# Kernel optimization log

Hardware: AMD Instinct MI355X
Metric: run time of the kernel (lower is better)

## Reference

```python
import jax, jax.numpy as jnp
import numpy as np

E = 2  # expand_ratio


def _linear_scan(u, a):
    """h_t = a_t * h_{t-1} + u_t along axis 0, h_{-1}=0. Parallel associative scan."""
    def comb(x, y):
        a1, b1 = x
        a2, b2 = y
        return a2 * a1, a2 * b1 + b2
    _, h = jax.lax.associative_scan(comb, (a, u), axis=0)
    return h


def setup_inputs() -> dict:
    key = jax.random.key(0)
    ks = jax.random.split(key, 8)
    n, b, d = 2048, 4, 1024
    s = 1.0 / np.sqrt(d)
    return {
        "x": jax.random.normal(ks[0], (n, b, d), jnp.float32),
        "lower_bound": jax.random.uniform(ks[1], (d,), jnp.float32),
        "W_in": jax.random.normal(ks[2], (d, 3 * d), jnp.float32) * s,
        "b_in": jnp.zeros((3 * d,), jnp.float32),
        "W_out": jax.random.normal(ks[3], (d, d), jnp.float32) * s,
        "b_out": jnp.zeros((d,), jnp.float32),
        "gamma": jnp.ones((d,), jnp.float32),
        "beta": jnp.zeros((d,), jnp.float32),
    }


def reference(x, lower_bound, W_in, b_in, W_out, b_out, gamma, beta):
    n, b, d = x.shape
    h = d // E
    feat = x @ W_in + b_in                      # (n,b,3d)
    inp, og, fg = jnp.split(feat, 3, axis=-1)
    inp = jax.nn.silu(inp)
    og = jax.nn.sigmoid(og)
    fg = jax.nn.sigmoid(fg)
    # reshape (h d) -> h, d=E
    inp = inp.reshape(n, b, h, E)
    og = og.reshape(n, b, h, E)
    fg = fg.reshape(n, b, h, E)
    lb = lower_bound.reshape(h, E)
    lam = lb + (1.0 - lb) * fg                  # (n,b,h,E)
    # outer-product input: (1-lam) outer inp over the E dims -> (n,b,h,E,E)
    u = jnp.einsum('nbhd,nbhe->nbhde', 1.0 - lam, inp)
    a = jnp.broadcast_to(lam[..., None], u.shape)
    u = u.reshape(n, b, h * E * E)
    a = a.reshape(n, b, h * E * E)
    state_fwd = _linear_scan(u, a)
    state_rev = jnp.flip(_linear_scan(jnp.flip(u, 0), jnp.flip(a, 0)), 0)
    state = (state_fwd + state_rev).reshape(n, b, h, E, E)
    out = jnp.einsum('nbhde,nbhd->nbhe', state, og).reshape(n, b, d)
    # layernorm over last dim
    mu = jnp.mean(out, axis=-1, keepdims=True)
    var = jnp.var(out, axis=-1, keepdims=True)
    out = (out - mu) * jax.lax.rsqrt(var + 1e-5) * gamma + beta
    return out @ W_out + b_out
```

## Files before the change

kernel.cpp:

```cpp
#include <hip/hip_runtime.h>

typedef __bf16 bf16x8 __attribute__((ext_vector_type(8)));
typedef float floatx4 __attribute__((ext_vector_type(4)));

#define NCH 128
#define CLEN 16

__device__ __forceinline__ unsigned short f2bf(float f) {
  unsigned int u = __builtin_bit_cast(unsigned int, f);
  u += 0x7fff + ((u >> 16) & 1);
  return (unsigned short)(u >> 16);
}
__device__ __forceinline__ float bf2f(unsigned short u) {
  unsigned int v = (unsigned int)u << 16;
  return __builtin_bit_cast(float, v);
}
__device__ __forceinline__ float bf2f_lo(unsigned int u) {
  return __builtin_bit_cast(float, u << 16);
}
__device__ __forceinline__ float bf2f_hi(unsigned int u) {
  return __builtin_bit_cast(float, u & 0xffff0000u);
}

__device__ __forceinline__ void async_copy16(const void* g, void* l) {
  __builtin_amdgcn_global_load_lds(
      (const __attribute__((address_space(1))) unsigned int*)g,
      (__attribute__((address_space(3))) unsigned int*)l, 16, 0, 0);
}

__global__ void cast_x_kernel(const float* __restrict__ in, unsigned short* __restrict__ out) {
  int i = blockIdx.x * blockDim.x + threadIdx.x;
  float4 v = ((const float4*)in)[i];
  ushort4 o;
  o.x = f2bf(v.x); o.y = f2bf(v.y); o.z = f2bf(v.z); o.w = f2bf(v.w);
  ((ushort4*)out)[i] = o;
}

__global__ void tcast2_kernel(const float* __restrict__ Win, unsigned short* __restrict__ winT,
                              const float* __restrict__ Wout, unsigned short* __restrict__ woutT) {
  __shared__ float tile[32][33];
  int bx = blockIdx.x;
  const float* W;
  unsigned short* WT;
  int ncols, n0;
  if (bx < 96) { W = Win; WT = winT; ncols = 3072; n0 = bx * 32; }
  else { W = Wout; WT = woutT; ncols = 1024; n0 = (bx - 96) * 32; }
  int k0 = blockIdx.y * 32;
  int tx = threadIdx.x, ty = threadIdx.y;
  tile[ty][tx] = W[(size_t)(k0 + ty) * ncols + n0 + tx];
  __syncthreads();
  WT[(size_t)(n0 + ty) * 1024 + k0 + tx] = f2bf(tile[tx][ty]);
}

template <int EPI>
__global__ __launch_bounds__(256) void gemm_kernel(
    const unsigned short* __restrict__ A, const unsigned short* __restrict__ BT,
    const float* __restrict__ bias, const float* __restrict__ lb,
    float* __restrict__ outf,
    unsigned short* __restrict__ o_inp, unsigned short* __restrict__ o_og,
    unsigned short* __restrict__ o_om) {
  __shared__ alignas(16) char smem_raw[17408];
  unsigned short* As = (unsigned short*)smem_raw;
  unsigned short* Bs = As + 128 * 32;
  const int m0 = blockIdx.x * 128, n0 = blockIdx.y * 128;
  const int tid = threadIdx.x;
  const int lane = tid & 63, wave = tid >> 6;
  const int wm = (wave >> 1) * 64, wn = (wave & 1) * 64;
  const int mrow = lane & 15, q = lane >> 4;
  const int qsw = q ^ ((mrow >> 1) & 3);
  floatx4 acc[4][4] = {};
  const int r0 = wave * 32;
  const int srow = r0 + (lane >> 2);
  const int qs = (lane & 3) ^ ((srow >> 1) & 3);
  const unsigned short* gA0 = A + (size_t)(m0 + srow) * 1024 + qs * 8;
  const unsigned short* gA1 = gA0 + (size_t)16 * 1024;
  const unsigned short* gB0 = BT + (size_t)(n0 + srow) * 1024 + qs * 8;
  const unsigned short* gB1 = gB0 + (size_t)16 * 1024;
  unsigned short* lA0 = &As[r0 * 32];
  unsigned short* lA1 = &As[(r0 + 16) * 32];
  unsigned short* lB0 = &Bs[r0 * 32];
  unsigned short* lB1 = &Bs[(r0 + 16) * 32];
  for (int kt = 0; kt < 1024; kt += 32) {
    __syncthreads();
    async_copy16(gA0, lA0);
    async_copy16(gA1, lA1);
    async_copy16(gB0, lB0);
    async_copy16(gB1, lB1);
    gA0 += 32; gA1 += 32; gB0 += 32; gB1 += 32;
    __syncthreads();
    bf16x8 af[4], bf[4];
#pragma unroll
    for (int i = 0; i < 4; i++) af[i] = *(const bf16x8*)&As[(wm + i * 16 + mrow) * 32 + qsw * 8];
#pragma unroll
    for (int j = 0; j < 4; j++) bf[j] = *(const bf16x8*)&Bs[(wn + j * 16 + mrow) * 32 + qsw * 8];
#pragma unroll
    for (int i = 0; i < 4; i++)
#pragma unroll
      for (int j = 0; j < 4; j++)
        acc[i][j] = __builtin_amdgcn_mfma_f32_16x16x32_bf16(af[i], bf[j], acc[i][j], 0, 0, 0);
  }
  const int er = tid >> 3;
  const int ec = (tid & 7) * 16;
  const int rgbase = m0 + (er & 15) + (er >> 4) * 64;
  const int lr = (wm ? 16 : 0) + q * 4;
  float bi[4];
  int cidx[4];
#pragma unroll
  for (int j = 0; j < 4; j++) {
    cidx[j] = n0 + wn + j * 16 + mrow;
    bi[j] = bias[cidx[j]];
  }
  if (EPI == 1) {
    unsigned short* Cs = (unsigned short*)smem_raw;
    const int seg = n0 >> 10;
    unsigned short* dst = (seg == 0) ? o_inp : (seg == 1) ? o_og : o_om;
    float Lv[4];
    if (seg == 2) {
#pragma unroll
      for (int j = 0; j < 4; j++) Lv[j] = lb[cidx[j] & 1023];
    }
#pragma unroll
    for (int i = 0; i < 4; i++) {
      __syncthreads();
#pragma unroll
      for (int j = 0; j < 4; j++) {
        const int lc = wn + j * 16 + mrow;
#pragma unroll
        for (int g = 0; g < 4; g++) {
          float v = acc[i][j][g] + bi[j];
          unsigned short ob;
          if (seg == 0) { float s = 1.f / (1.f + __expf(-v)); ob = f2bf(v * s); }
          else if (seg == 1) { float s = 1.f / (1.f + __expf(-v)); ob = f2bf(s); }
          else { float sm = 1.f / (1.f + __expf(v)); ob = f2bf((1.f - Lv[j]) * sm); }
          Cs[(lr + g) * 136 + lc] = ob;
        }
      }
      __syncthreads();
      uint4 v0 = *(uint4*)&Cs[er * 136 + ec];
      uint4 v1 = *(uint4*)&Cs[er * 136 + ec + 8];
      size_t ro = (size_t)(rgbase + i * 16) * 1024 + (n0 & 1023) + ec;
      *(uint4*)&dst[ro] = v0;
      *(uint4*)&dst[ro + 8] = v1;
    }
  } else {
    float* Cf = (float*)smem_raw;
#pragma unroll
    for (int i = 0; i < 4; i++) {
      __syncthreads();
#pragma unroll
      for (int j = 0; j < 4; j++) {
        const int lc = wn + j * 16 + mrow;
#pragma unroll
        for (int g = 0; g < 4; g++) Cf[(lr + g) * 132 + lc] = acc[i][j][g] + bi[j];
      }
      __syncthreads();
      size_t ro = (size_t)(rgbase + i * 16) * 1024 + n0 + ec;
#pragma unroll
      for (int k = 0; k < 4; k++) {
        float4 v = *(float4*)&Cf[er * 132 + ec + k * 4];
        *(float4*)&outf[ro + k * 4] = v;
      }
    }
  }
}

__global__ __launch_bounds__(512, 2) void gemm1_kernel(
    const unsigned short* __restrict__ A, const unsigned short* __restrict__ BT,
    const float* __restrict__ bias, const float* __restrict__ lb,
    unsigned short* __restrict__ o_inp, unsigned short* __restrict__ o_og,
    unsigned short* __restrict__ o_om) {
  __shared__ alignas(16) char smem[131072];
  const int orig = blockIdx.x;
  const int wg = (orig & 7) * 48 + (orig >> 3);
  const int m0 = (wg & 31) << 8;
  const int n0 = (wg >> 5) << 8;
  const int tid = threadIdx.x;
  const int lane = tid & 63, wave = tid >> 6;
  const int wm = wave >> 2, wn = wave & 3;
  const int srow = tid >> 3;
  const int sq = (tid & 7) ^ (srow & 7);
  const unsigned short* gA = A + (size_t)(m0 + srow) * 1024 + sq * 8;
  const unsigned short* gB = BT + (size_t)(n0 + srow) * 1024 + sq * 8;
  char* lw = smem + wave * 1024;
  const int aro = (wm * 128 + (lane & 15)) * 128;
  const int bro = (wn * 64 + (lane & 15)) * 128;
  const int qs0 = ((lane >> 4) ^ (lane & 7)) * 16;
  const int qs1 = ((4 + (lane >> 4)) ^ (lane & 7)) * 16;

  floatx4 acc[8][4] = {};
  bf16x8 aF[4][2], bF[4][2];

#define STG(lofs, gh, kk)                                \
  do {                                                   \
    const unsigned short* _g = (gh) + (size_t)(kk) * 64; \
    async_copy16(_g, lw + (lofs));                       \
    async_copy16(_g + 65536, lw + (lofs) + 8192);        \
  } while (0)
#define RA(base, mh, i, s) \
  (*(const bf16x8*)(smem + (base) + aro + (mh) * 8192 + (i) * 2048 + ((s) ? qs1 : qs0)))
#define RB(base, j, s) \
  (*(const bf16x8*)(smem + (base) + bro + (j) * 2048 + ((s) ? qs1 : qs0)))
#define BAR __builtin_amdgcn_s_barrier()
#define LGKM0 asm volatile("s_waitcnt lgkmcnt(0)" ::: "memory")
#define VM4 asm volatile("s_waitcnt vmcnt(4)" ::: "memory")
#define MM(d, a, b) d = __builtin_amdgcn_mfma_f32_16x16x32_bf16(a, b, d, 0, 0, 0)

  STG(65536, gB, 0);
  STG(65536 + 16384, gB + 131072, 0);
  STG(0, gA, 0);
  STG(0 + 16384, gA + 131072, 0);
  STG(98304, gB, 1);
  STG(98304 + 16384, gB + 131072, 1);
  VM4;
  BAR;

#pragma unroll 1
  for (int it = 0; it < 8; ++it) {
    const int t0 = 2 * it;
    const int kA1 = t0 + 1;
    const int kN2 = (t0 + 2 > 15) ? 15 : t0 + 2;
    const int kN3 = (t0 + 3 > 15) ? 15 : t0 + 3;
#pragma unroll
    for (int i = 0; i < 4; i++) { aF[i][0] = RA(0, 0, i, 0); aF[i][1] = RA(0, 0, i, 1); }
#pragma unroll
    for (int j = 0; j < 2; j++) { bF[j][0] = RB(65536, j, 0); bF[j][1] = RB(65536, j, 1); }
    STG(32768, gA, kA1);
    BAR; LGKM0;
    __builtin_amdgcn_s_setprio(1);
#pragma unroll
    for (int i = 0; i < 4; i++)
#pragma unroll
      for (int j = 0; j < 2; j++) { MM(acc[i][j], aF[i][0], bF[j][0]); MM(acc[i][j], aF[i][1], bF[j][1]); }
    __builtin_amdgcn_s_setprio(0);
    BAR;
#pragma unroll
    for (int j = 2; j < 4; j++) { bF[j][0] = RB(65536, j, 0); bF[j][1] = RB(65536, j, 1); }
    STG(32768 + 16384, gA + 131072, kA1);
    BAR; LGKM0;
    __builtin_amdgcn_s_setprio(1);
#pragma unroll
    for (int i = 0; i < 4; i++)
#pragma unroll
      for (int j = 2; j < 4; j++) { MM(acc[i][j], aF[i][0], bF[j][0]); MM(acc[i][j], aF[i][1], bF[j][1]); }
    __builtin_amdgcn_s_setprio(0);
    BAR;
#pragma unroll
    for (int i = 0; i < 4; i++) { aF[i][0] = RA(0, 1, i, 0); aF[i][1] = RA(0, 1, i, 1); }
    STG(65536, gB, kN2);
    BAR; LGKM0;
    __builtin_amdgcn_s_setprio(1);
#pragma unroll
    for (int i = 0; i < 4; i++)
#pragma unroll
      for (int j = 0; j < 2; j++) { MM(acc[4 + i][j], aF[i][0], bF[j][0]); MM(acc[4 + i][j], aF[i][1], bF[j][1]); }
    __builtin_amdgcn_s_setprio(0);
    BAR;
    STG(65536 + 16384, gB + 131072, kN2);
    BAR;
    __builtin_amdgcn_s_setprio(1);
#pragma unroll
    for (int i = 0; i < 4; i++)
#pragma unroll
      for (int j = 2; j < 4; j++) { MM(acc[4 + i][j], aF[i][0], bF[j][0]); MM(acc[4 + i][j], aF[i][1], bF[j][1]); }
    __builtin_amdgcn_s_setprio(0);
    VM4;
    BAR;
#pragma unroll
    for (int i = 0; i < 4; i++) { aF[i][0] = RA(32768, 0, i, 0); aF[i][1] = RA(32768, 0, i, 1); }
#pragma unroll
    for (int j = 0; j < 2; j++) { bF[j][0] = RB(98304, j, 0); bF[j][1] = RB(98304, j, 1); }
    STG(0, gA, kN2);
    BAR; LGKM0;
    __builtin_amdgcn_s_setprio(1);
#pragma unroll
    for (int i = 0; i < 4; i++)
#pragma unroll
      for (int j = 0; j < 2; j++) { MM(acc[i][j], aF[i][0], bF[j][0]); MM(acc[i][j], aF[i][1], bF[j][1]); }
    __builtin_amdgcn_s_setprio(0);
    BAR;
#pragma unroll
    for (int j = 2; j < 4; j++) { bF[j][0] = RB(98304, j, 0); bF[j][1] = RB(98304, j, 1); }
    STG(16384, gA + 131072, kN2);
    BAR; LGKM0;
    __builtin_amdgcn_s_setprio(1);
#pragma unroll
    for (int i = 0; i < 4; i++)
#pragma unroll
      for (int j = 2; j < 4; j++) { MM(acc[i][j], aF[i][0], bF[j][0]); MM(acc[i][j], aF[i][1], bF[j][1]); }
    __builtin_amdgcn_s_setprio(0);
    BAR;
#pragma unroll
    for (int i = 0; i < 4; i++) { aF[i][0] = RA(32768, 1, i, 0); aF[i][1] = RA(32768, 1, i, 1); }
    STG(98304, gB, kN3);
    BAR; LGKM0;
    __builtin_amdgcn_s_setprio(1);
#pragma unroll
    for (int i = 0; i < 4; i++)
#pragma unroll
      for (int j = 0; j < 2; j++) { MM(acc[4 + i][j], aF[i][0], bF[j][0]); MM(acc[4 + i][j], aF[i][1], bF[j][1]); }
    __builtin_amdgcn_s_setprio(0);
    BAR;
    STG(98304 + 16384, gB + 131072, kN3);
    BAR;
    __builtin_amdgcn_s_setprio(1);
#pragma unroll
    for (int i = 0; i < 4; i++)
#pragma unroll
      for (int j = 2; j < 4; j++) { MM(acc[4 + i][j], aF[i][0], bF[j][0]); MM(acc[4 + i][j], aF[i][1], bF[j][1]); }
    __builtin_amdgcn_s_setprio(0);
    VM4;
    BAR;
  }
#undef STG
#undef RA
#undef RB
#undef BAR
#undef LGKM0
#undef VM4
#undef MM

  asm volatile("s_waitcnt vmcnt(0) lgkmcnt(0)" ::: "memory");
  const int seg = n0 >> 10;
  unsigned short* dst = (seg == 0) ? o_inp : (seg == 1) ? o_og : o_om;
  unsigned short* Cs = (unsigned short*)smem;
  float bi[4], Lv[4];
#pragma unroll
  for (int j = 0; j < 4; j++) {
    const int c = n0 + wn * 64 + j * 16 + (lane & 15);
    bi[j] = bias[c];
    Lv[j] = (seg == 2) ? lb[c & 1023] : 0.f;
  }
  const int lrw = wm * 16 + (lane >> 4) * 4;
  const int lcw = wn * 64 + (lane & 15);
  const int er = tid >> 4, ec = (tid & 15) * 16;
  const int growb = m0 + (er >> 4) * 128 + (er & 15);
#pragma unroll
  for (int i = 0; i < 8; i++) {
    __syncthreads();
#pragma unroll
    for (int j = 0; j < 4; j++)
#pragma unroll
      for (int g = 0; g < 4; g++) {
        float v = acc[i][j][g] + bi[j];
        unsigned short ob;
        if (seg == 0) { float s = 1.f / (1.f + __expf(-v)); ob = f2bf(v * s); }
        else if (seg == 1) { float s = 1.f / (1.f + __expf(-v)); ob = f2bf(s); }
        else { float sm = 1.f / (1.f + __expf(v)); ob = f2bf((1.f - Lv[j]) * sm); }
        Cs[(lrw + g) * 264 + lcw + j * 16] = ob;
      }
    __syncthreads();
    uint4 v0 = *(uint4*)&Cs[er * 264 + ec];
    uint4 v1 = *(uint4*)&Cs[er * 264 + ec + 8];
    size_t ro = (size_t)(growb + i * 16) * 1024 + (n0 & 1023) + ec;
    *(uint4*)&dst[ro] = v0;
    *(uint4*)&dst[ro + 8] = v1;
  }
}

__global__ void scan_passA(const unsigned short* __restrict__ om, const unsigned short* __restrict__ ip,
                           float* __restrict__ sumA, float* __restrict__ sumBf,
                           float* __restrict__ sumBr) {
  int idx = blockIdx.x * 256 + threadIdx.x;
  int h = idx & 511, cb = idx >> 9, b = cb & 3, c = cb >> 2;
  long base = ((long)c * CLEN * 4 + b) * 1024 + 2 * h;
  float p0 = 1.f, p1 = 1.f;
  float s00 = 0.f, s01 = 0.f, s10 = 0.f, s11 = 0.f;
  float r00 = 0.f, r01 = 0.f, r10 = 0.f, r11 = 0.f;
#pragma unroll
  for (int t = 0; t < CLEN; t++) {
    ushort2 l2 = *(const ushort2*)(om + base);
    ushort2 i2 = *(const ushort2*)(ip + base);
    base += 4096;
    float omx = bf2f(l2.x), omy = bf2f(l2.y);
    float ipx = bf2f(i2.x), ipy = bf2f(i2.y);
    float lx = 1.f - omx, ly = 1.f - omy;
    float u00 = omx * ipx, u01 = omx * ipy, u10 = omy * ipx, u11 = omy * ipy;
    r00 += p0 * u00; r01 += p0 * u01; r10 += p1 * u10; r11 += p1 * u11;
    s00 = lx * s00 + u00; s01 = lx * s01 + u01;
    s10 = ly * s10 + u10; s11 = ly * s11 + u11;
    p0 *= lx; p1 *= ly;
  }
  ((float2*)sumA)[idx] = make_float2(p0, p1);
  ((float4*)sumBf)[idx] = make_float4(s00, s01, s10, s11);
  ((float4*)sumBr)[idx] = make_float4(r00, r01, r10, r11);
}

__global__ void scan_b1(const float* __restrict__ sumA, const float* __restrict__ sumBf,
                        const float* __restrict__ sumBr,
                        float* __restrict__ superA, float* __restrict__ superB) {
  int t = blockIdx.x * 256 + threadIdx.x;
  int ch = t & 3, bh = (t >> 2) & 2047, sc = (t >> 13) & 7, dir = t >> 16;
  int dd = ch >> 1;
  float Acc = 1.f, Bcc = 0.f;
  if (dir == 0) {
    for (int i = 0; i < 16; i++) {
      int si = (sc * 16 + i) * 2048 + bh;
      float a = sumA[(size_t)si * 2 + dd];
      float b = sumBf[(size_t)si * 4 + ch];
      Bcc = a * Bcc + b;
      Acc *= a;
    }
  } else {
    for (int i = 15; i >= 0; i--) {
      int si = (sc * 16 + i) * 2048 + bh;
      float a = sumA[(size_t)si * 2 + dd];
      float b = sumBr[(size_t)si * 4 + ch];
      Bcc = a * Bcc + b;
      Acc *= a;
    }
  }
  superA[t] = Acc;
  superB[t] = Bcc;
}

__global__ void scan_b2(const float* __restrict__ superA, const float* __restrict__ superB,
                        float* __restrict__ SI) {
  int t = blockIdx.x * 256 + threadIdx.x;
  int ch = t & 3, bh = (t >> 2) & 2047, dir = t >> 13;
  float H = 0.f;
  if (dir == 0) {
    for (int sc = 0; sc < 8; sc++) {
      size_t idx = ((size_t)(dir * 8 + sc) * 2048 + bh) * 4 + ch;
      SI[idx] = H;
      H = superA[idx] * H + superB[idx];
    }
  } else {
    for (int sc = 7; sc >= 0; sc--) {
      size_t idx = ((size_t)(dir * 8 + sc) * 2048 + bh) * 4 + ch;
      SI[idx] = H;
      H = superA[idx] * H + superB[idx];
    }
  }
}

__global__ void scan_b3(const float* __restrict__ sumA, const float* __restrict__ sumBf,
                        const float* __restrict__ sumBr, const float* __restrict__ SI,
                        float* __restrict__ initF, float* __restrict__ initR) {
  int t = blockIdx.x * 256 + threadIdx.x;
  int ch = t & 3, bh = (t >> 2) & 2047, sc = (t >> 13) & 7, dir = t >> 16;
  int dd = ch >> 1;
  float H = SI[t];
  if (dir == 0) {
    for (int i = 0; i < 16; i++) {
      int si = (sc * 16 + i) * 2048 + bh;
      initF[(size_t)si * 4 + ch] = H;
      H = sumA[(size_t)si * 2 + dd] * H + sumBf[(size_t)si * 4 + ch];
    }
  } else {
    for (int i = 15; i >= 0; i--) {
      int si = (sc * 16 + i) * 2048 + bh;
      initR[(size_t)si * 4 + ch] = H;
      H = sumA[(size_t)si * 2 + dd] * H + sumBr[(size_t)si * 4 + ch];
    }
  }
}

__global__ __launch_bounds__(512) void scanC_ln_kernel(
    const unsigned short* __restrict__ om, const unsigned short* __restrict__ ip,
    const unsigned short* __restrict__ og,
    const float* __restrict__ initF, const float* __restrict__ initR,
    const float* __restrict__ gamma, const float* __restrict__ beta,
    unsigned short* __restrict__ ybf) {
  __shared__ float tile[8][1024];
  __shared__ float ldsG[1024];
  __shared__ float ldsB[1024];
  const int h = threadIdx.x;
  const int cb = blockIdx.x;
  const int b = cb & 3, c = cb >> 2;
  const int idx = cb * 512 + h;
  *(float2*)&ldsG[2 * h] = *(const float2*)(gamma + 2 * h);
  *(float2*)&ldsB[2 * h] = *(const float2*)(beta + 2 * h);
  float4 F = ((const float4*)initF)[idx];
  float4 R = ((const float4*)initR)[idx];
  float outx[CLEN], outy[CLEN];
  unsigned int lS[CLEN], iS[CLEN], oS[CLEN];
  const long base = ((long)c * CLEN * 4 + b) * 1024 + 2 * h;
  float h00 = F.x, h01 = F.y, h10 = F.z, h11 = F.w;
  long p = base;
#pragma unroll
  for (int t = 0; t < CLEN; t++) {
    unsigned int l2 = *(const unsigned int*)(om + p);
    unsigned int i2 = *(const unsigned int*)(ip + p);
    unsigned int o2 = *(const unsigned int*)(og + p);
    p += 4096;
    lS[t] = l2; iS[t] = i2; oS[t] = o2;
    float omx = bf2f_lo(l2), omy = bf2f_hi(l2);
    float ipx = bf2f_lo(i2), ipy = bf2f_hi(i2);
    float ox = bf2f_lo(o2), oy = bf2f_hi(o2);
    float lx = 1.f - omx, ly = 1.f - omy;
    h00 = lx * h00 + omx * ipx; h01 = lx * h01 + omx * ipy;
    h10 = ly * h10 + omy * ipx; h11 = ly * h11 + omy * ipy;
    outx[t] = h00 * ox + h10 * oy;
    outy[t] = h01 * ox + h11 * oy;
  }
  float g00 = R.x, g01 = R.y, g10 = R.z, g11 = R.w;
#pragma unroll
  for (int t = CLEN - 1; t >= 0; t--) {
    unsigned int l2 = lS[t], i2 = iS[t], o2 = oS[t];
    float omx = bf2f_lo(l2), omy = bf2f_hi(l2);
    float ipx = bf2f_lo(i2), ipy = bf2f_hi(i2);
    float ox = bf2f_lo(o2), oy = bf2f_hi(o2);
    float lx = 1.f - omx, ly = 1.f - omy;
    g00 = omx * ipx + lx * g00; g01 = omx * ipy + lx * g01;
    g10 = omy * ipx + ly * g10; g11 = omy * ipy + ly * g11;
    outx[t] += g00 * ox + g10 * oy;
    outy[t] += g01 * ox + g11 * oy;
  }
  const int lane = h & 63, wv = h >> 6;
#pragma unroll
  for (int g = 0; g < CLEN / 8; g++) {
    __syncthreads();
#pragma unroll
    for (int r = 0; r < 8; r++) {
      float2 v2 = make_float2(outx[g * 8 + r], outy[g * 8 + r]);
      *(float2*)&tile[r][2 * h] = v2;
    }
    __syncthreads();
    {
      const int t = g * 8 + wv;
      float4 v[4];
#pragma unroll
      for (int k = 0; k < 4; k++) v[k] = *(const float4*)&tile[wv][lane * 16 + k * 4];
      float s = 0.f, s2 = 0.f;
#pragma unroll
      for (int k = 0; k < 4; k++) {
        s += v[k].x + v[k].y + v[k].z + v[k].w;
        s2 += v[k].x * v[k].x + v[k].y * v[k].y + v[k].z * v[k].z + v[k].w * v[k].w;
      }
#pragma unroll
      for (int off = 1; off < 64; off <<= 1) {
        s += __shfl_xor(s, off);
        s2 += __shfl_xor(s2, off);
      }
      float mean = s * (1.f / 1024.f);
      float var = s2 * (1.f / 1024.f) - mean * mean;
      float rstd = rsqrtf(var + 1e-5f);
      unsigned short o16[16];
#pragma unroll
      for (int k = 0; k < 4; k++) {
        float* vv = (float*)&v[k];
#pragma unroll
        for (int e = 0; e < 4; e++) {
          int ch = lane * 16 + k * 4 + e;
          o16[k * 4 + e] = f2bf((vv[e] - mean) * rstd * ldsG[ch] + ldsB[ch]);
        }
      }
      size_t rowo = ((size_t)(c * CLEN + t) * 4 + b) * 1024 + lane * 16;
      *(uint4*)(ybf + rowo) = *(uint4*)&o16[0];
      *(uint4*)(ybf + rowo + 8) = *(uint4*)&o16[8];
    }
  }
}

extern "C" void kernel_launch(void* const* d_in, const int* in_sizes, int n_in,
                              void* d_out, int out_size, void* d_ws, size_t ws_size,
                              hipStream_t stream) {
  const float* x = (const float*)d_in[0];
  const float* lb = (const float*)d_in[1];
  const float* Win = (const float*)d_in[2];
  const float* bin = (const float*)d_in[3];
  const float* Wout = (const float*)d_in[4];
  const float* bout = (const float*)d_in[5];
  const float* gamma = (const float*)d_in[6];
  const float* beta = (const float*)d_in[7];
  float* out = (float*)d_out;

  char* ws = (char*)d_ws;
  size_t off = 0;
  auto alloc = [&](size_t bytes) {
    void* p = ws + off;
    off += (bytes + 255) & ~(size_t)255;
    return p;
  };
  unsigned short* x_bf = (unsigned short*)alloc(8192ull * 1024 * 2);
  unsigned short* winT = (unsigned short*)alloc(3072ull * 1024 * 2);
  unsigned short* woutT = (unsigned short*)alloc(1024ull * 1024 * 2);
  unsigned short* inp_b = (unsigned short*)alloc(8192ull * 1024 * 2);
  unsigned short* og_b = (unsigned short*)alloc(8192ull * 1024 * 2);
  unsigned short* om_b = (unsigned short*)alloc(8192ull * 1024 * 2);
  unsigned short* y_bf = (unsigned short*)alloc(8192ull * 1024 * 2);
  float* sumA = (float*)alloc((size_t)NCH * 4 * 512 * 2 * 4);
  float* sumBf = (float*)alloc((size_t)NCH * 4 * 512 * 4 * 4);
  float* sumBr = (float*)alloc((size_t)NCH * 4 * 512 * 4 * 4);
  float* initF = (float*)alloc((size_t)NCH * 4 * 512 * 4 * 4);
  float* initR = (float*)alloc((size_t)NCH * 4 * 512 * 4 * 4);
  float* superA = (float*)alloc(131072ull * 4);
  float* superB = (float*)alloc(131072ull * 4);
  float* SIbuf = (float*)alloc(131072ull * 4);

  cast_x_kernel<<<8192, 256, 0, stream>>>(x, x_bf);
  tcast2_kernel<<<dim3(128, 32), dim3(32, 32), 0, stream>>>(Win, winT, Wout, woutT);
  gemm1_kernel<<<384, 512, 0, stream>>>(x_bf, winT, bin, lb, inp_b, og_b, om_b);
  scan_passA<<<(NCH * 4 * 512) / 256, 256, 0, stream>>>(om_b, inp_b, sumA, sumBf, sumBr);
  scan_b1<<<512, 256, 0, stream>>>(sumA, sumBf, sumBr, superA, superB);
  scan_b2<<<64, 256, 0, stream>>>(superA, superB, SIbuf);
  scan_b3<<<512, 256, 0, stream>>>(sumA, sumBf, sumBr, SIbuf, initF, initR);
  scanC_ln_kernel<<<NCH * 4, 512, 0, stream>>>(om_b, inp_b, og_b, initF, initR, gamma, beta, y_bf);
  gemm_kernel<0><<<dim3(64, 8), 256, 0, stream>>>(y_bf, woutT, bout, nullptr, out, nullptr, nullptr, nullptr);
}
```

Baseline: 261.8 us.

## Shrink gemm1 tile to 128x256 with triple-buffered LDS pipeline

New measurement: 245.8 us. 1.06x faster.

```diff
diff --git a/kernel.cpp b/kernel.cpp
--- a/kernel.cpp
+++ b/kernel.cpp
@@ -169,11 +169,11 @@
     const float* __restrict__ bias, const float* __restrict__ lb,
     unsigned short* __restrict__ o_inp, unsigned short* __restrict__ o_og,
     unsigned short* __restrict__ o_om) {
-  __shared__ alignas(16) char smem[131072];
+  __shared__ alignas(16) char smem[147456];
   const int orig = blockIdx.x;
-  const int wg = (orig & 7) * 48 + (orig >> 3);
-  const int m0 = (wg & 31) << 8;
-  const int n0 = (wg >> 5) << 8;
+  const int wg = (orig & 7) * 96 + (orig >> 3);
+  const int m0 = (wg & 63) << 7;
+  const int n0 = (wg >> 6) << 8;
   const int tid = threadIdx.x;
   const int lane = tid & 63, wave = tid >> 6;
   const int wm = wave >> 2, wn = wave & 3;
@@ -182,12 +182,12 @@
   const unsigned short* gA = A + (size_t)(m0 + srow) * 1024 + sq * 8;
   const unsigned short* gB = BT + (size_t)(n0 + srow) * 1024 + sq * 8;
   char* lw = smem + wave * 1024;
-  const int aro = (wm * 128 + (lane & 15)) * 128;
+  const int aro = (wm * 64 + (lane & 15)) * 128;
   const int bro = (wn * 64 + (lane & 15)) * 128;
   const int qs0 = ((lane >> 4) ^ (lane & 7)) * 16;
   const int qs1 = ((4 + (lane >> 4)) ^ (lane & 7)) * 16;
 
-  floatx4 acc[8][4] = {};
+  floatx4 acc[4][4] = {};
   bf16x8 aF[4][2], bF[4][2];
 
 #define STG(lofs, gh, kk)                                \
@@ -196,128 +196,73 @@
     async_copy16(_g, lw + (lofs));                       \
     async_copy16(_g + 65536, lw + (lofs) + 8192);        \
   } while (0)
-#define RA(base, mh, i, s) \
-  (*(const bf16x8*)(smem + (base) + aro + (mh) * 8192 + (i) * 2048 + ((s) ? qs1 : qs0)))
+#define RA(base, i, s) \
+  (*(const bf16x8*)(smem + (base) + aro + (i) * 2048 + ((s) ? qs1 : qs0)))
 #define RB(base, j, s) \
   (*(const bf16x8*)(smem + (base) + bro + (j) * 2048 + ((s) ? qs1 : qs0)))
 #define BAR __builtin_amdgcn_s_barrier()
 #define LGKM0 asm volatile("s_waitcnt lgkmcnt(0)" ::: "memory")
-#define VM4 asm volatile("s_waitcnt vmcnt(4)" ::: "memory")
+#define VM6 asm volatile("s_waitcnt vmcnt(6)" ::: "memory")
 #define MM(d, a, b) d = __builtin_amdgcn_mfma_f32_16x16x32_bf16(a, b, d, 0, 0, 0)
 
-  STG(65536, gB, 0);
-  STG(65536 + 16384, gB + 131072, 0);
+#define TILE(AB, BB, SA, SB, kk)                                               \
+  do {                                                                         \
+    _Pragma("unroll") for (int i = 0; i < 4; i++) {                            \
+      aF[i][0] = RA(AB, i, 0); aF[i][1] = RA(AB, i, 1);                        \
+    }                                                                          \
+    _Pragma("unroll") for (int j = 0; j < 2; j++) {                            \
+      bF[j][0] = RB(BB, j, 0); bF[j][1] = RB(BB, j, 1);                        \
+    }                                                                          \
+    STG(SA, gA, kk);                                                           \
+    STG(SB, gB, kk);                                                           \
+    BAR; LGKM0;                                                                \
+    __builtin_amdgcn_s_setprio(1);                                             \
+    _Pragma("unroll") for (int i = 0; i < 4; i++) {                            \
+      _Pragma("unroll") for (int j = 0; j < 2; j++) {                          \
+        MM(acc[i][j], aF[i][0], bF[j][0]); MM(acc[i][j], aF[i][1], bF[j][1]);  \
+      }                                                                        \
+    }                                                                          \
+    __builtin_amdgcn_s_setprio(0);                                             \
+    BAR;                                                                       \
+    _Pragma("unroll") for (int j = 2; j < 4; j++) {                            \
+      bF[j][0] = RB(BB, j, 0); bF[j][1] = RB(BB, j, 1);                        \
+    }                                                                          \
+    STG((SB) + 16384, gB + 131072, kk);                                        \
+    BAR; LGKM0;                                                                \
+    __builtin_amdgcn_s_setprio(1);                                             \
+    _Pragma("unroll") for (int i = 0; i < 4; i++) {                            \
+      _Pragma("unroll") for (int j = 2; j < 4; j++) {                          \
+        MM(acc[i][j], aF[i][0], bF[j][0]); MM(acc[i][j], aF[i][1], bF[j][1]);  \
+      }                                                                        \
+    }                                                                          \
+    __builtin_amdgcn_s_setprio(0);                                             \
+    VM6; BAR;                                                                  \
+  } while (0)
+
   STG(0, gA, 0);
-  STG(0 + 16384, gA + 131072, 0);
-  STG(98304, gB, 1);
-  STG(98304 + 16384, gB + 131072, 1);
-  VM4;
+  STG(49152, gB, 0);
+  STG(49152 + 16384, gB + 131072, 0);
+  STG(16384, gA, 1);
+  STG(81920, gB, 1);
+  STG(81920 + 16384, gB + 131072, 1);
+  VM6;
   BAR;
 
 #pragma unroll 1
-  for (int it = 0; it < 8; ++it) {
-    const int t0 = 2 * it;
-    const int kA1 = t0 + 1;
-    const int kN2 = (t0 + 2 > 15) ? 15 : t0 + 2;
-    const int kN3 = (t0 + 3 > 15) ? 15 : t0 + 3;
-#pragma unroll
-    for (int i = 0; i < 4; i++) { aF[i][0] = RA(0, 0, i, 0); aF[i][1] = RA(0, 0, i, 1); }
-#pragma unroll
-    for (int j = 0; j < 2; j++) { bF[j][0] = RB(65536, j, 0); bF[j][1] = RB(65536, j, 1); }
-    STG(32768, gA, kA1);
-    BAR; LGKM0;
-    __builtin_amdgcn_s_setprio(1);
-#pragma unroll
-    for (int i = 0; i < 4; i++)
-#pragma unroll
-      for (int j = 0; j < 2; j++) { MM(acc[i][j], aF[i][0], bF[j][0]); MM(acc[i][j], aF[i][1], bF[j][1]); }
-    __builtin_amdgcn_s_setprio(0);
-    BAR;
-#pragma unroll
-    for (int j = 2; j < 4; j++) { bF[j][0] = RB(65536, j, 0); bF[j][1] = RB(65536, j, 1); }
-    STG(32768 + 16384, gA + 131072, kA1);
-    BAR; LGKM0;
-    __builtin_amdgcn_s_setprio(1);
-#pragma unroll
-    for (int i = 0; i < 4; i++)
-#pragma unroll
-      for (int j = 2; j < 4; j++) { MM(acc[i][j], aF[i][0], bF[j][0]); MM(acc[i][j], aF[i][1], bF[j][1]); }
-    __builtin_amdgcn_s_setprio(0);
-    BAR;
-#pragma unroll
-    for (int i = 0; i < 4; i++) { aF[i][0] = RA(0, 1, i, 0); aF[i][1] = RA(0, 1, i, 1); }
-    STG(65536, gB, kN2);
-    BAR; LGKM0;
-    __builtin_amdgcn_s_setprio(1);
-#pragma unroll
-    for (int i = 0; i < 4; i++)
-#pragma unroll
-      for (int j = 0; j < 2; j++) { MM(acc[4 + i][j], aF[i][0], bF[j][0]); MM(acc[4 + i][j], aF[i][1], bF[j][1]); }
-    __builtin_amdgcn_s_setprio(0);
-    BAR;
-    STG(65536 + 16384, gB + 131072, kN2);
-    BAR;
-    __builtin_amdgcn_s_setprio(1);
-#pragma unroll
-    for (int i = 0; i < 4; i++)
-#pragma unroll
-      for (int j = 2; j < 4; j++) { MM(acc[4 + i][j], aF[i][0], bF[j][0]); MM(acc[4 + i][j], aF[i][1], bF[j][1]); }
-    __builtin_amdgcn_s_setprio(0);
-    VM4;
-    BAR;
-#pragma unroll
-    for (int i = 0; i < 4; i++) { aF[i][0] = RA(32768, 0, i, 0); aF[i][1] = RA(32768, 0, i, 1); }
-#pragma unroll
-    for (int j = 0; j < 2; j++) { bF[j][0] = RB(98304, j, 0); bF[j][1] = RB(98304, j, 1); }
-    STG(0, gA, kN2);
-    BAR; LGKM0;
-    __builtin_amdgcn_s_setprio(1);
-#pragma unroll
-    for (int i = 0; i < 4; i++)
-#pragma unroll
-      for (int j = 0; j < 2; j++) { MM(acc[i][j], aF[i][0], bF[j][0]); MM(acc[i][j], aF[i][1], bF[j][1]); }
-    __builtin_amdgcn_s_setprio(0);
-    BAR;
-#pragma unroll
-    for (int j = 2; j < 4; j++) { bF[j][0] = RB(98304, j, 0); bF[j][1] = RB(98304, j, 1); }
-    STG(16384, gA + 131072, kN2);
-    BAR; LGKM0;
-    __builtin_amdgcn_s_setprio(1);
-#pragma unroll
-    for (int i = 0; i < 4; i++)
-#pragma unroll
-      for (int j = 2; j < 4; j++) { MM(acc[i][j], aF[i][0], bF[j][0]); MM(acc[i][j], aF[i][1], bF[j][1]); }
-    __builtin_amdgcn_s_setprio(0);
-    BAR;
-#pragma unroll
-    for (int i = 0; i < 4; i++) { aF[i][0] = RA(32768, 1, i, 0); aF[i][1] = RA(32768, 1, i, 1); }
-    STG(98304, gB, kN3);
-    BAR; LGKM0;
-    __builtin_amdgcn_s_setprio(1);
-#pragma unroll
-    for (int i = 0; i < 4; i++)
-#pragma unroll
-      for (int j = 0; j < 2; j++) { MM(acc[4 + i][j], aF[i][0], bF[j][0]); MM(acc[4 + i][j], aF[i][1], bF[j][1]); }
-    __builtin_amdgcn_s_setprio(0);
-    BAR;
-    STG(98304 + 16384, gB + 131072, kN3);
-    BAR;
-    __builtin_amdgcn_s_setprio(1);
-#pragma unroll
-    for (int i = 0; i < 4; i++)
-#pragma unroll
-      for (int j = 2; j < 4; j++) { MM(acc[4 + i][j], aF[i][0], bF[j][0]); MM(acc[4 + i][j], aF[i][1], bF[j][1]); }
-    __builtin_amdgcn_s_setprio(0);
-    VM4;
-    BAR;
-  }
+  for (int tt = 0; tt < 15; tt += 3) {
+    TILE(0, 49152, 32768, 114688, tt + 2);
+    TILE(16384, 81920, 0, 49152, tt + 3);
+    TILE(32768, 114688, 16384, 81920, (tt + 4 > 15 ? 15 : tt + 4));
+  }
+  TILE(0, 49152, 32768, 114688, 15);
 #undef STG
 #undef RA
 #undef RB
 #undef BAR
 #undef LGKM0
-#undef VM4
+#undef VM6
 #undef MM
+#undef TILE
 
   asm volatile("s_waitcnt vmcnt(0) lgkmcnt(0)" ::: "memory");
   const int seg = n0 >> 10;
@@ -333,9 +278,9 @@
   const int lrw = wm * 16 + (lane >> 4) * 4;
   const int lcw = wn * 64 + (lane & 15);
   const int er = tid >> 4, ec = (tid & 15) * 16;
-  const int growb = m0 + (er >> 4) * 128 + (er & 15);
-#pragma unroll
-  for (int i = 0; i < 8; i++) {
+  const int growb = m0 + (er >> 4) * 64 + (er & 15);
+#pragma unroll
+  for (int i = 0; i < 4; i++) {
     __syncthreads();
 #pragma unroll
     for (int j = 0; j < 4; j++)
@@ -590,7 +535,7 @@
 
   cast_x_kernel<<<8192, 256, 0, stream>>>(x, x_bf);
   tcast2_kernel<<<dim3(128, 32), dim3(32, 32), 0, stream>>>(Win, winT, Wout, woutT);
-  gemm1_kernel<<<384, 512, 0, stream>>>(x_bf, winT, bin, lb, inp_b, og_b, om_b);
+  gemm1_kernel<<<768, 512, 0, stream>>>(x_bf, winT, bin, lb, inp_b, og_b, om_b);
   scan_passA<<<(NCH * 4 * 512) / 256, 256, 0, stream>>>(om_b, inp_b, sumA, sumBf, sumBr);
   scan_b1<<<512, 256, 0, stream>>>(sumA, sumBf, sumBr, superA, superB);
   scan_b2<<<64, 256, 0, stream>>>(superA, superB, SIbuf);
```
